# Optimization experiments

Measured on AMD Instinct MI355X. Metric: run time of the kernel, lower is better.

## Reference

```python
import jax, jax.numpy as jnp
import numpy as np

N_NODES = 10000
N_EDGES = 160000
D = 512
DROPOUT_P = 0.5
NEG_SLOPE = 0.25


def setup_inputs() -> dict:
    key = jax.random.key(0)
    ks = jax.random.split(key, 8)
    H = jax.random.normal(ks[0], (N_NODES, D), dtype=jnp.float32)
    rows = jax.random.randint(ks[1], (N_EDGES,), 0, N_NODES)
    cols = jax.random.randint(ks[2], (N_EDGES,), 0, N_NODES)
    vals = jax.random.uniform(ks[3], (N_EDGES,), dtype=jnp.float32)
    # xavier-normal-ish weights, zero bias (matches torch init)
    std = float(np.sqrt(2.0 / (D + D)))
    W1 = jax.random.normal(ks[4], (D, D), dtype=jnp.float32) * std
    b1 = jnp.zeros((D,), dtype=jnp.float32)
    W2 = jax.random.normal(ks[5], (D, D), dtype=jnp.float32) * std
    b2 = jnp.zeros((D,), dtype=jnp.float32)
    return {"H": H, "rows": rows, "cols": cols, "vals": vals,
            "W1": W1, "b1": b1, "W2": W2, "b2": b2}


def _spmm(rows, cols, vals, dense):
    # sparse [N,N] @ dense [N,D] via gather + segment-sum
    gathered = vals[:, None] * dense[cols]          # [E, D]
    return jax.ops.segment_sum(gathered, rows, num_segments=N_NODES)


def _leaky_relu(x):
    return jnp.where(x >= 0, x, NEG_SLOPE * x)


def reference(H, rows, cols, vals, W1, b1, W2, b2):
    # layer 1: dense GEMM -> SpMM -> bias -> leaky_relu -> dropout(training=True)
    h = _spmm(rows, cols, vals, H @ W1) + b1
    h = _leaky_relu(h)
    keep = jax.random.bernoulli(jax.random.key(42), 1.0 - DROPOUT_P, h.shape)
    h = jnp.where(keep, h / (1.0 - DROPOUT_P), 0.0)
    # layer 2
    h = _spmm(rows, cols, vals, h @ W2) + b2
    return _leaky_relu(h)
```

## Files before the change

kernel.cpp:

```cpp
#include <hip/hip_runtime.h>
#include <stdint.h>

#define N_NODES 10000
#define M_PAD   10112
#define N_EDGES 160000
#define DIM     512
#define N_ELEMS 5120000
#define NEG_SLOPE 0.25f
#define ELL_W   64

typedef short          short8   __attribute__((ext_vector_type(8)));
typedef unsigned short ushort8v __attribute__((ext_vector_type(8)));
typedef __bf16         bf16x8   __attribute__((ext_vector_type(8)));
typedef float          f32x4    __attribute__((ext_vector_type(4)));

__device__ __forceinline__ unsigned short f2bf(float f) {
    uint32_t u = __builtin_bit_cast(uint32_t, f);
    uint32_t r = (u + 0x7fffu + ((u >> 16) & 1u)) >> 16;
    return (unsigned short)r;
}
__device__ __forceinline__ float b2f(unsigned short u) {
    return __builtin_bit_cast(float, (uint32_t)u << 16);
}

__device__ __forceinline__ uint32_t rotl32(uint32_t x, uint32_t d) {
    return (x << d) | (x >> (32u - d));
}
__device__ __forceinline__ void threefry_42(uint32_t x0, uint32_t x1,
                                            uint32_t& o0, uint32_t& o1) {
    const uint32_t ks0 = 0u, ks1 = 42u, ks2 = 0x1BD11BDAu ^ 42u;
    x0 += ks0; x1 += ks1;
#define TF_R4(a,b,c,d) \
    x0 += x1; x1 = rotl32(x1,a); x1 ^= x0; \
    x0 += x1; x1 = rotl32(x1,b); x1 ^= x0; \
    x0 += x1; x1 = rotl32(x1,c); x1 ^= x0; \
    x0 += x1; x1 = rotl32(x1,d); x1 ^= x0;
    TF_R4(13,15,26,6);  x0 += ks1; x1 += ks2 + 1u;
    TF_R4(17,29,16,24); x0 += ks2; x1 += ks0 + 2u;
    TF_R4(13,15,26,6);  x0 += ks0; x1 += ks1 + 3u;
    TF_R4(17,29,16,24); x0 += ks1; x1 += ks2 + 4u;
    TF_R4(13,15,26,6);  x0 += ks2; x1 += ks0 + 5u;
#undef TF_R4
    o0 = x0; o1 = x1;
}

#define CONV_BLKS 5000
#define TR_BLKS   64
#define ZERO_BLKS 10

__device__ __forceinline__ void transpose_tile(const float* __restrict__ W,
                                               unsigned short* __restrict__ WT,
                                               int tile, float (*ts)[65]) {
    int k0 = (tile & 7) * 64, n0 = (tile >> 3) * 64;
    int tx = threadIdx.x & 15, ty = threadIdx.x >> 4;
    #pragma unroll
    for (int i = 0; i < 4; ++i) {
        int k = i * 16 + ty;
        float4 v = *(const float4*)&W[(size_t)(k0 + k) * DIM + n0 + tx * 4];
        ts[k][tx * 4 + 0] = v.x; ts[k][tx * 4 + 1] = v.y;
        ts[k][tx * 4 + 2] = v.z; ts[k][tx * 4 + 3] = v.w;
    }
    __syncthreads();
    #pragma unroll
    for (int i = 0; i < 4; ++i) {
        int n = i * 16 + ty;
        ushort4 o;
        o.x = f2bf(ts[tx * 4 + 0][n]); o.y = f2bf(ts[tx * 4 + 1][n]);
        o.z = f2bf(ts[tx * 4 + 2][n]); o.w = f2bf(ts[tx * 4 + 3][n]);
        *(ushort4*)&WT[(size_t)(n0 + n) * DIM + k0 + tx * 4] = o;
    }
}

__global__ __launch_bounds__(256)
void prep_kernel(const float* __restrict__ H, const float* __restrict__ W1,
                 const float* __restrict__ W2, unsigned short* __restrict__ Abf,
                 unsigned short* __restrict__ WT1, unsigned short* __restrict__ WT2,
                 int* __restrict__ deg) {
    __shared__ float ts[64][65];
    int b = blockIdx.x;
    if (b < CONV_BLKS) {
        int i = b * 256 + threadIdx.x;
        float4 v = ((const float4*)H)[i];
        ushort4 o;
        o.x = f2bf(v.x); o.y = f2bf(v.y); o.z = f2bf(v.z); o.w = f2bf(v.w);
        ((ushort4*)Abf)[i] = o;
    } else if (b < CONV_BLKS + TR_BLKS) {
        transpose_tile(W1, WT1, b - CONV_BLKS, ts);
    } else if (b < CONV_BLKS + 2 * TR_BLKS) {
        transpose_tile(W2, WT2, b - CONV_BLKS - TR_BLKS, ts);
    } else {
        int i = (b - CONV_BLKS - 2 * TR_BLKS) * 1024 + threadIdx.x * 4;
        #pragma unroll
        for (int j = 0; j < 4; ++j)
            if (i + j < N_NODES) deg[i + j] = 0;
    }
}

__global__ void ell_scatter(const int* __restrict__ rows, const int* __restrict__ cols,
                            const float* __restrict__ vals, int* __restrict__ deg,
                            int2* __restrict__ epack) {
    int e = blockIdx.x * blockDim.x + threadIdx.x;
    if (e < N_EDGES) {
        int r = rows[e];
        int p = atomicAdd(&deg[r], 1);
        epack[(size_t)r * ELL_W + p] = make_int2(cols[e], __float_as_int(vals[e]));
    }
}

__global__ __launch_bounds__(256)
void mfma_gemm(const unsigned short* __restrict__ A, const unsigned short* __restrict__ BT,
               unsigned short* __restrict__ C, int M) {
    __shared__ short8 As[1024];
    __shared__ short8 Bs[1024];
    int tid  = threadIdx.x;
    int wid  = tid >> 6, lane = tid & 63;
    int bm   = blockIdx.x * 128;
    int bn   = blockIdx.y * 128;
    int wm   = (wid >> 1) * 64, wn = (wid & 1) * 64;

    f32x4 acc[4][4] = {};
    int srow = lane >> 3;
    int sslot = lane & 7;

    for (int k0 = 0; k0 < DIM; k0 += 64) {
        #pragma unroll
        for (int c = 0; c < 4; ++c) {
            int chunk = wid * 4 + c;
            int r  = chunk * 8 + srow;
            int ks = sslot ^ (r & 7);
            const unsigned short* ga = A  + (size_t)(bm + r) * DIM + k0 + ks * 8;
            const unsigned short* gb = BT + (size_t)(bn + r) * DIM + k0 + ks * 8;
            __builtin_amdgcn_global_load_lds(
                (const __attribute__((address_space(1))) void*)ga,
                (__attribute__((address_space(3))) void*)&As[chunk * 64], 16, 0, 0);
            __builtin_amdgcn_global_load_lds(
                (const __attribute__((address_space(1))) void*)gb,
                (__attribute__((address_space(3))) void*)&Bs[chunk * 64], 16, 0, 0);
        }
        __syncthreads();

        int lrow = lane & 15;
        int kgrp = lane >> 4;
        #pragma unroll
        for (int ks = 0; ks < 2; ++ks) {
            short8 af[4], bfr[4];
            #pragma unroll
            for (int i = 0; i < 4; ++i) {
                int r = wm + i * 16 + lrow;
                af[i]  = As[r * 8 + ((ks * 4 + kgrp) ^ (r & 7))];
                int n = wn + i * 16 + lrow;
                bfr[i] = Bs[n * 8 + ((ks * 4 + kgrp) ^ (n & 7))];
            }
            #pragma unroll
            for (int i = 0; i < 4; ++i)
                #pragma unroll
                for (int j = 0; j < 4; ++j)
                    acc[i][j] = __builtin_amdgcn_mfma_f32_16x16x32_bf16(
                        __builtin_bit_cast(bf16x8, af[i]),
                        __builtin_bit_cast(bf16x8, bfr[j]), acc[i][j], 0, 0, 0);
        }
        __syncthreads();
    }

    int crow = (lane >> 4) * 4;
    int ccol = lane & 15;
    #pragma unroll
    for (int i = 0; i < 4; ++i) {
        #pragma unroll
        for (int r = 0; r < 4; ++r) {
            int row = bm + wm + i * 16 + crow + r;
            if (row < M) {
                size_t base = (size_t)row * DIM + bn + wn + ccol;
                #pragma unroll
                for (int j = 0; j < 4; ++j)
                    C[base + j * 16] = f2bf(acc[i][j][r]);
            }
        }
    }
}

template <int LAYER>
__global__ __launch_bounds__(128)
void spmm_kernel(const unsigned short* __restrict__ X, const int* __restrict__ deg,
                 const int2* __restrict__ epack, const float* __restrict__ bias,
                 void* __restrict__ outp) {
    __shared__ float part[2][DIM];
    int row  = blockIdx.x;
    int w    = threadIdx.x >> 6;
    int lane = threadIdx.x & 63;
    int d = deg[row];
    const int2* ep = epack + (size_t)row * ELL_W;
    const ushort8v* X8 = (const ushort8v*)X;

    float acc[8] = {};
    int base = w * 8;
    for (; base + 8 <= d; base += 16) {
        int4 e01 = *(const int4*)(ep + base);
        int4 e23 = *(const int4*)(ep + base + 2);
        int4 e45 = *(const int4*)(ep + base + 4);
        int4 e67 = *(const int4*)(ep + base + 6);
        ushort8v x0 = X8[(size_t)e01.x * 64 + lane];
        ushort8v x1 = X8[(size_t)e01.z * 64 + lane];
        ushort8v x2 = X8[(size_t)e23.x * 64 + lane];
        ushort8v x3 = X8[(size_t)e23.z * 64 + lane];
        ushort8v x4 = X8[(size_t)e45.x * 64 + lane];
        ushort8v x5 = X8[(size_t)e45.z * 64 + lane];
        ushort8v x6 = X8[(size_t)e67.x * 64 + lane];
        ushort8v x7 = X8[(size_t)e67.z * 64 + lane];
        float v0 = __int_as_float(e01.y), v1 = __int_as_float(e01.w);
        float v2 = __int_as_float(e23.y), v3 = __int_as_float(e23.w);
        float v4 = __int_as_float(e45.y), v5 = __int_as_float(e45.w);
        float v6 = __int_as_float(e67.y), v7 = __int_as_float(e67.w);
        #pragma unroll
        for (int j = 0; j < 8; ++j) {
            acc[j] = fmaf(v0, b2f(x0[j]), acc[j]);
            acc[j] = fmaf(v1, b2f(x1[j]), acc[j]);
            acc[j] = fmaf(v2, b2f(x2[j]), acc[j]);
            acc[j] = fmaf(v3, b2f(x3[j]), acc[j]);
            acc[j] = fmaf(v4, b2f(x4[j]), acc[j]);
            acc[j] = fmaf(v5, b2f(x5[j]), acc[j]);
            acc[j] = fmaf(v6, b2f(x6[j]), acc[j]);
            acc[j] = fmaf(v7, b2f(x7[j]), acc[j]);
        }
    }
    int tail_end = base + 8 < d ? base + 8 : d;
    for (int s = base; s < tail_end; ++s) {
        int2 e = ep[s];
        ushort8v x = X8[(size_t)e.x * 64 + lane];
        float v = __int_as_float(e.y);
        #pragma unroll
        for (int j = 0; j < 8; ++j) acc[j] = fmaf(v, b2f(x[j]), acc[j]);
    }

    #pragma unroll
    for (int j = 0; j < 8; ++j) part[w][j * 64 + lane] = acc[j];
    __syncthreads();

    int t = threadIdx.x;
    float4 b = *(const float4*)&bias[t * 4];
    float bb[4] = { b.x, b.y, b.z, b.w };
    float r[4];
    #pragma unroll
    for (int j = 0; j < 4; ++j) {
        int c = t * 4 + j;
        int idx = (c & 7) * 64 + (c >> 3);
        float v = part[0][idx] + part[1][idx] + bb[j];
        r[j] = (v >= 0.f) ? v : NEG_SLOPE * v;
    }
    if (LAYER == 1) {
        uint32_t e0 = (uint32_t)row * DIM + t * 4;
        ushort4 o;
        #pragma unroll
        for (int j = 0; j < 4; ++j) {
            uint32_t o0, o1;
            threefry_42(0u, e0 + j, o0, o1);
            uint32_t bits = o0 ^ o1;
            float v = ((int)bits >= 0) ? r[j] * 2.0f : 0.0f;
            ((unsigned short*)&o)[j] = f2bf(v);
        }
        ((ushort4*)outp)[(size_t)row * 128 + t] = o;
    } else {
        float4 o = make_float4(r[0], r[1], r[2], r[3]);
        ((float4*)outp)[(size_t)row * 128 + t] = o;
    }
}

extern "C" void kernel_launch(void* const* d_in, const int* in_sizes, int n_in,
                              void* d_out, int out_size, void* d_ws, size_t ws_size,
                              hipStream_t stream) {
    const float* H    = (const float*)d_in[0];
    const int*   rows = (const int*)  d_in[1];
    const int*   cols = (const int*)  d_in[2];
    const float* vals = (const float*)d_in[3];
    const float* W1   = (const float*)d_in[4];
    const float* b1   = (const float*)d_in[5];
    const float* W2   = (const float*)d_in[6];
    const float* b2   = (const float*)d_in[7];
    float* out = (float*)d_out;

    char* ws = (char*)d_ws;
    size_t off = 0;
    auto alloc = [&](size_t bytes) -> void* {
        off = (off + 255) & ~(size_t)255;
        void* p = ws + off;
        off += bytes;
        return p;
    };
    int*  deg   = (int*) alloc((size_t)N_NODES * 4);
    int2* epack = (int2*)alloc((size_t)N_NODES * ELL_W * 8);
    unsigned short* WT1 = (unsigned short*)alloc((size_t)DIM * DIM * 2);
    unsigned short* WT2 = (unsigned short*)alloc((size_t)DIM * DIM * 2);
    unsigned short* Abf = (unsigned short*)alloc((size_t)M_PAD * DIM * 2);
    unsigned short* hbf = (unsigned short*)alloc((size_t)M_PAD * DIM * 2);
    unsigned short* Xbf = (unsigned short*)alloc((size_t)N_NODES * DIM * 2);

    int prep_blocks = CONV_BLKS + 2 * TR_BLKS + ZERO_BLKS;
    prep_kernel<<<prep_blocks, 256, 0, stream>>>(H, W1, W2, Abf, WT1, WT2, deg);
    ell_scatter<<<(N_EDGES + 255) / 256, 256, 0, stream>>>(rows, cols, vals, deg, epack);

    dim3 ggrid(M_PAD / 128, DIM / 128);
    mfma_gemm<<<ggrid, 256, 0, stream>>>(Abf, WT1, Xbf, N_NODES);
    spmm_kernel<1><<<N_NODES, 128, 0, stream>>>(Xbf, deg, epack, b1, hbf);
    mfma_gemm<<<ggrid, 256, 0, stream>>>(hbf, WT2, Xbf, N_NODES);
    spmm_kernel<2><<<N_NODES, 128, 0, stream>>>(Xbf, deg, epack, b2, out);
}
```

Measured before the change: 106.8 us.

## Map one wavefront per row in SpMM and zero-pad ELL to remove tail loop

Each SpMM block now handles four rows, one wavefront per row, so the shared-memory partial-sum reduction and the block barrier go away. The ELL edge buffer is zero-filled in the prep kernel, so rows can be processed in padded groups of 8 without a scalar tail loop, with 16 edges unrolled per iteration. The cost is an extra 5 MB memory write during prep, less parallelism per row, and wasted gathers on padded slots.

```diff
diff --git a/kernel.cpp b/kernel.cpp
--- a/kernel.cpp
+++ b/kernel.cpp
@@ -46,6 +46,7 @@
 
 #define CONV_BLKS 5000
 #define TR_BLKS   64
+#define EZ_BLKS   1250
 #define ZERO_BLKS 10
 
 __device__ __forceinline__ void transpose_tile(const float* __restrict__ W,
@@ -75,7 +76,7 @@
 void prep_kernel(const float* __restrict__ H, const float* __restrict__ W1,
                  const float* __restrict__ W2, unsigned short* __restrict__ Abf,
                  unsigned short* __restrict__ WT1, unsigned short* __restrict__ WT2,
-                 int* __restrict__ deg) {
+                 int4* __restrict__ epack4, int* __restrict__ deg) {
     __shared__ float ts[64][65];
     int b = blockIdx.x;
     if (b < CONV_BLKS) {
@@ -88,8 +89,11 @@
         transpose_tile(W1, WT1, b - CONV_BLKS, ts);
     } else if (b < CONV_BLKS + 2 * TR_BLKS) {
         transpose_tile(W2, WT2, b - CONV_BLKS - TR_BLKS, ts);
+    } else if (b < CONV_BLKS + 2 * TR_BLKS + EZ_BLKS) {
+        int i = (b - CONV_BLKS - 2 * TR_BLKS) * 256 + threadIdx.x;
+        epack4[i] = make_int4(0, 0, 0, 0);
     } else {
-        int i = (b - CONV_BLKS - 2 * TR_BLKS) * 1024 + threadIdx.x * 4;
+        int i = (b - CONV_BLKS - 2 * TR_BLKS - EZ_BLKS) * 1024 + threadIdx.x * 4;
         #pragma unroll
         for (int j = 0; j < 4; ++j)
             if (i + j < N_NODES) deg[i + j] = 0;
@@ -180,37 +184,52 @@
 }
 
 template <int LAYER>
-__global__ __launch_bounds__(128)
+__global__ __launch_bounds__(256)
 void spmm_kernel(const unsigned short* __restrict__ X, const int* __restrict__ deg,
                  const int2* __restrict__ epack, const float* __restrict__ bias,
                  void* __restrict__ outp) {
-    __shared__ float part[2][DIM];
-    int row  = blockIdx.x;
-    int w    = threadIdx.x >> 6;
+    int row  = blockIdx.x * 4 + (threadIdx.x >> 6);
     int lane = threadIdx.x & 63;
-    int d = deg[row];
+    int d  = deg[row];
+    int dp = (d + 7) & ~7;
     const int2* ep = epack + (size_t)row * ELL_W;
     const ushort8v* X8 = (const ushort8v*)X;
 
     float acc[8] = {};
-    int base = w * 8;
-    for (; base + 8 <= d; base += 16) {
-        int4 e01 = *(const int4*)(ep + base);
-        int4 e23 = *(const int4*)(ep + base + 2);
-        int4 e45 = *(const int4*)(ep + base + 4);
-        int4 e67 = *(const int4*)(ep + base + 6);
-        ushort8v x0 = X8[(size_t)e01.x * 64 + lane];
-        ushort8v x1 = X8[(size_t)e01.z * 64 + lane];
-        ushort8v x2 = X8[(size_t)e23.x * 64 + lane];
-        ushort8v x3 = X8[(size_t)e23.z * 64 + lane];
-        ushort8v x4 = X8[(size_t)e45.x * 64 + lane];
-        ushort8v x5 = X8[(size_t)e45.z * 64 + lane];
-        ushort8v x6 = X8[(size_t)e67.x * 64 + lane];
-        ushort8v x7 = X8[(size_t)e67.z * 64 + lane];
-        float v0 = __int_as_float(e01.y), v1 = __int_as_float(e01.w);
-        float v2 = __int_as_float(e23.y), v3 = __int_as_float(e23.w);
-        float v4 = __int_as_float(e45.y), v5 = __int_as_float(e45.w);
-        float v6 = __int_as_float(e67.y), v7 = __int_as_float(e67.w);
+    int base = 0;
+    for (; base + 16 <= dp; base += 16) {
+        int4 eA = *(const int4*)(ep + base);
+        int4 eB = *(const int4*)(ep + base + 2);
+        int4 eC = *(const int4*)(ep + base + 4);
+        int4 eD = *(const int4*)(ep + base + 6);
+        int4 eE = *(const int4*)(ep + base + 8);
+        int4 eF = *(const int4*)(ep + base + 10);
+        int4 eG = *(const int4*)(ep + base + 12);
+        int4 eH = *(const int4*)(ep + base + 14);
+        ushort8v x0 = X8[(size_t)eA.x * 64 + lane];
+        ushort8v x1 = X8[(size_t)eA.z * 64 + lane];
+        ushort8v x2 = X8[(size_t)eB.x * 64 + lane];
+        ushort8v x3 = X8[(size_t)eB.z * 64 + lane];
+        ushort8v x4 = X8[(size_t)eC.x * 64 + lane];
+        ushort8v x5 = X8[(size_t)eC.z * 64 + lane];
+        ushort8v x6 = X8[(size_t)eD.x * 64 + lane];
+        ushort8v x7 = X8[(size_t)eD.z * 64 + lane];
+        ushort8v x8 = X8[(size_t)eE.x * 64 + lane];
+        ushort8v x9 = X8[(size_t)eE.z * 64 + lane];
+        ushort8v xa = X8[(size_t)eF.x * 64 + lane];
+        ushort8v xb = X8[(size_t)eF.z * 64 + lane];
+        ushort8v xc = X8[(size_t)eG.x * 64 + lane];
+        ushort8v xd = X8[(size_t)eG.z * 64 + lane];
+        ushort8v xe = X8[(size_t)eH.x * 64 + lane];
+        ushort8v xf = X8[(size_t)eH.z * 64 + lane];
+        float v0 = __int_as_float(eA.y), v1 = __int_as_float(eA.w);
+        float v2 = __int_as_float(eB.y), v3 = __int_as_float(eB.w);
+        float v4 = __int_as_float(eC.y), v5 = __int_as_float(eC.w);
+        float v6 = __int_as_float(eD.y), v7 = __int_as_float(eD.w);
+        float v8 = __int_as_float(eE.y), v9 = __int_as_float(eE.w);
+        float va = __int_as_float(eF.y), vb = __int_as_float(eF.w);
+        float vc = __int_as_float(eG.y), vd = __int_as_float(eG.w);
+        float ve = __int_as_float(eH.y), vf = __int_as_float(eH.w);
         #pragma unroll
         for (int j = 0; j < 8; ++j) {
             acc[j] = fmaf(v0, b2f(x0[j]), acc[j]);
@@ -221,47 +240,72 @@
             acc[j] = fmaf(v5, b2f(x5[j]), acc[j]);
             acc[j] = fmaf(v6, b2f(x6[j]), acc[j]);
             acc[j] = fmaf(v7, b2f(x7[j]), acc[j]);
-        }
-    }
-    int tail_end = base + 8 < d ? base + 8 : d;
-    for (int s = base; s < tail_end; ++s) {
-        int2 e = ep[s];
-        ushort8v x = X8[(size_t)e.x * 64 + lane];
-        float v = __int_as_float(e.y);
-        #pragma unroll
-        for (int j = 0; j < 8; ++j) acc[j] = fmaf(v, b2f(x[j]), acc[j]);
-    }
-
+            acc[j] = fmaf(v8, b2f(x8[j]), acc[j]);
+            acc[j] = fmaf(v9, b2f(x9[j]), acc[j]);
+            acc[j] = fmaf(va, b2f(xa[j]), acc[j]);
+            acc[j] = fmaf(vb, b2f(xb[j]), acc[j]);
+            acc[j] = fmaf(vc, b2f(xc[j]), acc[j]);
+            acc[j] = fmaf(vd, b2f(xd[j]), acc[j]);
+            acc[j] = fmaf(ve, b2f(xe[j]), acc[j]);
+            acc[j] = fmaf(vf, b2f(xf[j]), acc[j]);
+        }
+    }
+    if (base < dp) {
+        int4 eA = *(const int4*)(ep + base);
+        int4 eB = *(const int4*)(ep + base + 2);
+        int4 eC = *(const int4*)(ep + base + 4);
+        int4 eD = *(const int4*)(ep + base + 6);
+        ushort8v x0 = X8[(size_t)eA.x * 64 + lane];
+        ushort8v x1 = X8[(size_t)eA.z * 64 + lane];
+        ushort8v x2 = X8[(size_t)eB.x * 64 + lane];
+        ushort8v x3 = X8[(size_t)eB.z * 64 + lane];
+        ushort8v x4 = X8[(size_t)eC.x * 64 + lane];
+        ushort8v x5 = X8[(size_t)eC.z * 64 + lane];
+        ushort8v x6 = X8[(size_t)eD.x * 64 + lane];
+        ushort8v x7 = X8[(size_t)eD.z * 64 + lane];
+        float v0 = __int_as_float(eA.y), v1 = __int_as_float(eA.w);
+        float v2 = __int_as_float(eB.y), v3 = __int_as_float(eB.w);
+        float v4 = __int_as_float(eC.y), v5 = __int_as_float(eC.w);
+        float v6 = __int_as_float(eD.y), v7 = __int_as_float(eD.w);
+        #pragma unroll
+        for (int j = 0; j < 8; ++j) {
+            acc[j] = fmaf(v0, b2f(x0[j]), acc[j]);
+            acc[j] = fmaf(v1, b2f(x1[j]), acc[j]);
+            acc[j] = fmaf(v2, b2f(x2[j]), acc[j]);
+            acc[j] = fmaf(v3, b2f(x3[j]), acc[j]);
+            acc[j] = fmaf(v4, b2f(x4[j]), acc[j]);
+            acc[j] = fmaf(v5, b2f(x5[j]), acc[j]);
+            acc[j] = fmaf(v6, b2f(x6[j]), acc[j]);
+            acc[j] = fmaf(v7, b2f(x7[j]), acc[j]);
+        }
+    }
+
+    float4 bi0 = ((const float4*)bias)[lane * 2];
+    float4 bi1 = ((const float4*)bias)[lane * 2 + 1];
+    float bb[8] = { bi0.x, bi0.y, bi0.z, bi0.w, bi1.x, bi1.y, bi1.z, bi1.w };
+    float r[8];
     #pragma unroll
-    for (int j = 0; j < 8; ++j) part[w][j * 64 + lane] = acc[j];
-    __syncthreads();
-
-    int t = threadIdx.x;
-    float4 b = *(const float4*)&bias[t * 4];
-    float bb[4] = { b.x, b.y, b.z, b.w };
-    float r[4];
-    #pragma unroll
-    for (int j = 0; j < 4; ++j) {
-        int c = t * 4 + j;
-        int idx = (c & 7) * 64 + (c >> 3);
-        float v = part[0][idx] + part[1][idx] + bb[j];
+    for (int j = 0; j < 8; ++j) {
+        float v = acc[j] + bb[j];
         r[j] = (v >= 0.f) ? v : NEG_SLOPE * v;
     }
     if (LAYER == 1) {
-        uint32_t e0 = (uint32_t)row * DIM + t * 4;
-        ushort4 o;
-        #pragma unroll
-        for (int j = 0; j < 4; ++j) {
+        uint32_t e0 = (uint32_t)row * DIM + lane * 8;
+        ushort8v o;
+        #pragma unroll
+        for (int j = 0; j < 8; ++j) {
             uint32_t o0, o1;
             threefry_42(0u, e0 + j, o0, o1);
             uint32_t bits = o0 ^ o1;
             float v = ((int)bits >= 0) ? r[j] * 2.0f : 0.0f;
-            ((unsigned short*)&o)[j] = f2bf(v);
-        }
-        ((ushort4*)outp)[(size_t)row * 128 + t] = o;
+            o[j] = f2bf(v);
+        }
+        ((ushort8v*)outp)[(size_t)row * 64 + lane] = o;
     } else {
-        float4 o = make_float4(r[0], r[1], r[2], r[3]);
-        ((float4*)outp)[(size_t)row * 128 + t] = o;
+        float4 o0 = make_float4(r[0], r[1], r[2], r[3]);
+        float4 o1 = make_float4(r[4], r[5], r[6], r[7]);
+        ((float4*)outp)[(size_t)row * 128 + lane * 2]     = o0;
+        ((float4*)outp)[(size_t)row * 128 + lane * 2 + 1] = o1;
     }
 }
 
@@ -294,13 +338,14 @@
     unsigned short* hbf = (unsigned short*)alloc((size_t)M_PAD * DIM * 2);
     unsigned short* Xbf = (unsigned short*)alloc((size_t)N_NODES * DIM * 2);
 
-    int prep_blocks = CONV_BLKS + 2 * TR_BLKS + ZERO_BLKS;
-    prep_kernel<<<prep_blocks, 256, 0, stream>>>(H, W1, W2, Abf, WT1, WT2, deg);
+    int prep_blocks = CONV_BLKS + 2 * TR_BLKS + EZ_BLKS + ZERO_BLKS;
+    prep_kernel<<<prep_blocks, 256, 0, stream>>>(H, W1, W2, Abf, WT1, WT2,
+                                                 (int4*)epack, deg);
     ell_scatter<<<(N_EDGES + 255) / 256, 256, 0, stream>>>(rows, cols, vals, deg, epack);
 
     dim3 ggrid(M_PAD / 128, DIM / 128);
     mfma_gemm<<<ggrid, 256, 0, stream>>>(Abf, WT1, Xbf, N_NODES);
-    spmm_kernel<1><<<N_NODES, 128, 0, stream>>>(Xbf, deg, epack, b1, hbf);
+    spmm_kernel<1><<<N_NODES / 4, 256, 0, stream>>>(Xbf, deg, epack, b1, hbf);
     mfma_gemm<<<ggrid, 256, 0, stream>>>(hbf, WT2, Xbf, N_NODES);
-    spmm_kernel<2><<<N_NODES, 128, 0, stream>>>(Xbf, deg, epack, b2, out);
-}
+    spmm_kernel<2><<<N_NODES / 4, 256, 0, stream>>>(Xbf, deg, epack, b2, out);
+}
```

Result: faster. 102.2 us (median of 2 runs) (-4.3%).
